# Kernel optimization log

Measured on AMD Instinct MI355X. Metric: run time of the kernel, lower is better.

Reference implementation:

```python
import jax, jax.numpy as jnp
import numpy as np


def setup_inputs() -> dict:
    key = jax.random.key(0)
    k1, k2, k3, k4, k5 = jax.random.split(key, 5)
    B, T, N, F_IN, F_OUT, N_TYPES = 32, 128, 32, 256, 256, 8
    inp = jax.random.normal(k1, (B, T, N, F_IN), dtype=jnp.float32)
    g = jax.random.uniform(k2, (N, N), dtype=jnp.float32)
    node_type_index = jax.random.randint(k3, (N,), 0, N_TYPES, dtype=jnp.int64 if jax.config.read('jax_enable_x64') else jnp.int32)
    weight = jax.random.normal(k4, (N_TYPES, F_OUT, F_IN), dtype=jnp.float32) * (1.0 / np.sqrt(F_IN))
    bias = jax.random.normal(k5, (N_TYPES, F_OUT), dtype=jnp.float32) * 0.01
    return {"input": inp, "g": g, "node_type_index": node_type_index,
            "weight": weight, "bias": bias}


def reference(input, g, node_type_index, weight, bias):
    # Gather per-node weights/biases by node type.
    w = weight[node_type_index]            # [N, out, in]
    b = bias[node_type_index]              # [N, out]
    # Per-node linear: out[..., n, o] = sum_i input[..., n, i] * w[n, o, i]
    out = jnp.einsum('btni,noi->btno', input, w) + b  # [B, T, N, out]
    # Graph aggregation over node dim: g [N, N] @ out [..., N, out]
    out = jnp.einsum('mn,btno->btmo', g, out)
    return out
```

## Files before the change

kernel.cpp:

```cpp
#include <hip/hip_runtime.h>
#include <hip/hip_bf16.h>
#include <stdint.h>

typedef __bf16 bf16x8 __attribute__((ext_vector_type(8)));
typedef __bf16 bf16x4 __attribute__((ext_vector_type(4)));
typedef float f32x4 __attribute__((ext_vector_type(4)));

#define N_NODES 32
#define FDIM 256
#define N_TYPES 8
#define BT_TILE 32
#define TILES 16
#define ROW_B (FDIM * 2)

__device__ __forceinline__ unsigned swz(unsigned byte_off, unsigned row) {
    return byte_off ^ ((row & 7u) << 4);
}
__device__ __forceinline__ void lds_dma16(void* lds, const void* g) {
    __builtin_amdgcn_global_load_lds(
        (const __attribute__((address_space(1))) unsigned int*)g,
        (__attribute__((address_space(3))) unsigned int*)lds, 16, 0, 0);
}

__global__ __launch_bounds__(256) void k0_convert_w(
    const float* __restrict__ w, __bf16* __restrict__ wp)
{
    int idx = blockIdx.x * 256 + threadIdx.x;
    int t = idx >> 16, o = (idx >> 8) & 255, k = idx & 255;
    unsigned L = (unsigned)(o * ROW_B + k * 2) ^ ((o & 7u) << 4);
    wp[(size_t)t * (FDIM * FDIM) + (L >> 1)] = (__bf16)w[idx];
}

__global__ __launch_bounds__(256, 1) void k1_node_gemm(
    const float* __restrict__ input, const __bf16* __restrict__ wp,
    const float* __restrict__ bias, const int* __restrict__ ntype,
    char* __restrict__ outb)
{
    __shared__ __bf16 sW[FDIM * FDIM];
    __shared__ __bf16 sA[2][BT_TILE * FDIM];

    const int tid = threadIdx.x;
    const int n = blockIdx.x >> 3;
    const int base = (blockIdx.x & 7) * (TILES * BT_TILE);
    const int t = ntype[n];

    const int wid = tid >> 6, lane = tid & 63;
    const int lr = lane & 15, lq = lane >> 4;
    const int sr = tid >> 3;
    const int sk = tid & 7;

    char* sWb = (char*)sW;
    char* sA0 = (char*)sA[0];
    char* sA1 = (char*)sA[1];

    const char* wsrc = (const char*)(wp + (size_t)t * (FDIM * FDIM));
#pragma unroll
    for (int j = 0; j < 32; ++j)
        lds_dma16(sWb + j * 4096 + tid * 16, wsrc + j * 4096 + tid * 16);

    float bv[4];
#pragma unroll
    for (int nf = 0; nf < 4; ++nf)
        bv[nf] = bias[t * FDIM + wid * 64 + nf * 16 + lr];

    const char* Abase = (const char*)input
        + ((size_t)(base + sr) * (N_NODES * FDIM) + n * FDIM) * 4 + sk * 16;
    const size_t tile_stride = (size_t)BT_TILE * N_NODES * FDIM * 4;

    float4 av0[8], av1[8];
#pragma unroll
    for (int q = 0; q < 8; ++q)
        av0[q] = *reinterpret_cast<const float4*>(Abase + q * 128);
#pragma unroll
    for (int q = 0; q < 8; ++q)
        av1[q] = *reinterpret_cast<const float4*>(Abase + tile_stride + q * 128);

#pragma unroll
    for (int q = 0; q < 8; ++q) {
        bf16x4 h; h[0]=(__bf16)av0[q].x; h[1]=(__bf16)av0[q].y;
        h[2]=(__bf16)av0[q].z; h[3]=(__bf16)av0[q].w;
        *reinterpret_cast<bf16x4*>(sA0 + swz(sr * ROW_B + q * 64 + sk * 8, sr)) = h;
    }
    __syncthreads();

    f32x4 acc[2][4];

#define COMPUTE_TILE(SBUF, TI)                                                  \
    {                                                                           \
        _Pragma("unroll")                                                       \
        for (int mf = 0; mf < 2; ++mf)                                          \
            _Pragma("unroll")                                                   \
            for (int nf = 0; nf < 4; ++nf)                                      \
                acc[mf][nf] = f32x4{0.f, 0.f, 0.f, 0.f};                        \
        _Pragma("unroll")                                                       \
        for (int ks = 0; ks < 8; ++ks) {                                        \
            const int kb = ks * 64 + lq * 16;                                   \
            bf16x8 af[2], bfv[4];                                               \
            _Pragma("unroll")                                                   \
            for (int mf = 0; mf < 2; ++mf) {                                    \
                int r = mf * 16 + lr;                                           \
                af[mf] = *reinterpret_cast<const bf16x8*>(                      \
                    SBUF + swz(r * ROW_B + kb, r));                             \
            }                                                                   \
            _Pragma("unroll")                                                   \
            for (int nf = 0; nf < 4; ++nf) {                                    \
                int o = wid * 64 + nf * 16 + lr;                                \
                bfv[nf] = *reinterpret_cast<const bf16x8*>(                     \
                    sWb + swz(o * ROW_B + kb, o));                              \
            }                                                                   \
            _Pragma("unroll")                                                   \
            for (int mf = 0; mf < 2; ++mf)                                      \
                _Pragma("unroll")                                               \
                for (int nf = 0; nf < 4; ++nf)                                  \
                    acc[mf][nf] = __builtin_amdgcn_mfma_f32_16x16x32_bf16(      \
                        af[mf], bfv[nf], acc[mf][nf], 0, 0, 0);                 \
        }                                                                       \
                  \
        _Pragma("unroll")                                                       \
        for (int mf = 0; mf < 2; ++mf)                                          \
            _Pragma("unroll")                                                   \
            for (int j = 0; j < 4; ++j) {                                       \
                bf16x4 h;                                                       \
                _Pragma("unroll")                                               \
                for (int nf = 0; nf < 4; ++nf)                                  \
                    h[nf] = (__bf16)(acc[mf][nf][j] + bv[nf]);                  \
                size_t bt = (size_t)(base + (TI) * BT_TILE + mf * 16 + lq * 4 + j); \
                *reinterpret_cast<bf16x4*>(outb + bt * 32768 + n * 512          \
                                           + wid * 128 + lr * 8) = h;           \
            }                                                                   \
    }

#define CVT_TO(AV, SDST)                                                        \
    {                                                                           \
        _Pragma("unroll")                                                       \
        for (int q = 0; q < 8; ++q) {                                           \
            bf16x4 h; h[0]=(__bf16)AV[q].x; h[1]=(__bf16)AV[q].y;               \
            h[2]=(__bf16)AV[q].z; h[3]=(__bf16)AV[q].w;                         \
            *reinterpret_cast<bf16x4*>(SDST + swz(sr * ROW_B + q * 64 + sk * 8, \
                                                  sr)) = h;                     \
        }                                                                       \
    }

#define LOAD_TILE(AV, TI)                                                       \
    {                                                                           \
        const char* rp = Abase + (size_t)(TI) * tile_stride;                    \
        _Pragma("unroll")                                                       \
        for (int q = 0; q < 8; ++q)                                             \
            AV[q] = *reinterpret_cast<const float4*>(rp + q * 128);             \
    }

    for (int tt = 0; tt < 8; ++tt) {
        const int e = 2 * tt;
        if (e + 2 < TILES) LOAD_TILE(av0, e + 2);
        COMPUTE_TILE(sA0, e);
        CVT_TO(av1, sA1);
        __syncthreads();
        const int od = 2 * tt + 1;
        if (od + 2 < TILES) LOAD_TILE(av1, od + 2);
        COMPUTE_TILE(sA1, od);
        if (tt < 7) {
            CVT_TO(av0, sA0);
            __syncthreads();
        }
    }
#undef COMPUTE_TILE
#undef CVT_TO
#undef LOAD_TILE
}

__global__ __launch_bounds__(256) void k2_graph_agg(
    char* __restrict__ outb, const float* __restrict__ g)
{
    const int tid = threadIdx.x;
    const int bt = blockIdx.x;
    const int o = tid;
    const unsigned pb = ((unsigned)(o >> 6) << 7) + ((o & 15u) << 3)
                      + (((o >> 4) & 3u) << 1);

    const char* src = outb + (size_t)bt * 32768 + pb;
    float v[N_NODES];
#pragma unroll
    for (int nn = 0; nn < N_NODES; ++nn) {
        unsigned short hv = *reinterpret_cast<const unsigned short*>(src + nn * 512);
        union { unsigned u; float f; } cv; cv.u = (unsigned)hv << 16;
        v[nn] = cv.f;
    }
    __syncthreads();

    float* dst = (float*)(outb + (size_t)bt * 32768) + o;
#pragma unroll 4
    for (int m = 0; m < N_NODES; ++m) {
        float s = 0.f;
#pragma unroll
        for (int nn = 0; nn < N_NODES; ++nn)
            s = fmaf(g[m * N_NODES + nn], v[nn], s);
        dst[m * FDIM] = s;
    }
}

extern "C" void kernel_launch(void* const* d_in, const int* in_sizes, int n_in,
                              void* d_out, int out_size, void* d_ws, size_t ws_size,
                              hipStream_t stream) {
    const float* input  = (const float*)d_in[0];
    const float* g      = (const float*)d_in[1];
    const int*   ntype  = (const int*)d_in[2];
    const float* weight = (const float*)d_in[3];
    const float* bias   = (const float*)d_in[4];
    char* outb = (char*)d_out;
    __bf16* wp = (__bf16*)d_ws;

    const int BT = in_sizes[0] / (N_NODES * FDIM);

    k0_convert_w<<<N_TYPES * FDIM * FDIM / 256, 256, 0, stream>>>(weight, wp);

    k1_node_gemm<<<N_NODES * 8, 256, 0, stream>>>(input, wp, bias, ntype, outb);

    k2_graph_agg<<<BT, 256, 0, stream>>>(outb, g);
}
```

Measured before the change: 82.92 us.

## Store fp32 node-GEMM intermediate in output and stage g in LDS

The node GEMM now writes its fp32 results straight into the output buffer in natural layout, replacing the packed bf16 intermediate. The graph aggregation kernel reads float2 pairs, handles two BT rows per block, and caches g in shared memory instead of reading it from global memory on every FMA. This doubles the intermediate write and read traffic, since fp32 replaces bf16, but removes the bf16 rounding and gives coalesced vector access. The k1 stores are scalar, strided by 16 floats per lane group, which may coalesce less well than the old bf16x4 stores.

```diff
diff --git a/kernel.cpp b/kernel.cpp
--- a/kernel.cpp
+++ b/kernel.cpp
@@ -34,7 +34,7 @@
 __global__ __launch_bounds__(256, 1) void k1_node_gemm(
     const float* __restrict__ input, const __bf16* __restrict__ wp,
     const float* __restrict__ bias, const int* __restrict__ ntype,
-    char* __restrict__ outb)
+    float* __restrict__ outf)
 {
     __shared__ __bf16 sW[FDIM * FDIM];
     __shared__ __bf16 sA[2][BT_TILE * FDIM];
@@ -115,18 +115,17 @@
                     acc[mf][nf] = __builtin_amdgcn_mfma_f32_16x16x32_bf16(      \
                         af[mf], bfv[nf], acc[mf][nf], 0, 0, 0);                 \
         }                                                                       \
-                  \
+                          \
         _Pragma("unroll")                                                       \
         for (int mf = 0; mf < 2; ++mf)                                          \
             _Pragma("unroll")                                                   \
             for (int j = 0; j < 4; ++j) {                                       \
-                bf16x4 h;                                                       \
+                size_t bt = (size_t)(base + (TI) * BT_TILE + mf * 16 + lq * 4 + j); \
+                float* orow = outf + bt * (N_NODES * FDIM) + n * FDIM           \
+                              + wid * 64 + lr;                                  \
                 _Pragma("unroll")                                               \
                 for (int nf = 0; nf < 4; ++nf)                                  \
-                    h[nf] = (__bf16)(acc[mf][nf][j] + bv[nf]);                  \
-                size_t bt = (size_t)(base + (TI) * BT_TILE + mf * 16 + lq * 4 + j); \
-                *reinterpret_cast<bf16x4*>(outb + bt * 32768 + n * 512          \
-                                           + wid * 128 + lr * 8) = h;           \
+                    orow[nf * 16] = acc[mf][nf][j] + bv[nf];                    \
             }                                                                   \
     }
 
@@ -169,32 +168,32 @@
 }
 
 __global__ __launch_bounds__(256) void k2_graph_agg(
-    char* __restrict__ outb, const float* __restrict__ g)
+    float* __restrict__ out, const float* __restrict__ g)
 {
+    __shared__ float gs[N_NODES * N_NODES];
     const int tid = threadIdx.x;
-    const int bt = blockIdx.x;
-    const int o = tid;
-    const unsigned pb = ((unsigned)(o >> 6) << 7) + ((o & 15u) << 3)
-                      + (((o >> 4) & 3u) << 1);
-
-    const char* src = outb + (size_t)bt * 32768 + pb;
-    float v[N_NODES];
-#pragma unroll
-    for (int nn = 0; nn < N_NODES; ++nn) {
-        unsigned short hv = *reinterpret_cast<const unsigned short*>(src + nn * 512);
-        union { unsigned u; float f; } cv; cv.u = (unsigned)hv << 16;
-        v[nn] = cv.f;
-    }
+    reinterpret_cast<float4*>(gs)[tid] = reinterpret_cast<const float4*>(g)[tid];
+
+    const size_t bt = (size_t)blockIdx.x * 2 + (tid >> 7);
+    const int oc = tid & 127;
+    float2* base = reinterpret_cast<float2*>(out + bt * (N_NODES * FDIM)) + oc;
+
+    float2 v[N_NODES];
+#pragma unroll
+    for (int nn = 0; nn < N_NODES; ++nn)
+        v[nn] = base[nn * (FDIM / 2)];
     __syncthreads();
 
-    float* dst = (float*)(outb + (size_t)bt * 32768) + o;
 #pragma unroll 4
     for (int m = 0; m < N_NODES; ++m) {
-        float s = 0.f;
-#pragma unroll
-        for (int nn = 0; nn < N_NODES; ++nn)
-            s = fmaf(g[m * N_NODES + nn], v[nn], s);
-        dst[m * FDIM] = s;
+        float sx = 0.f, sy = 0.f;
+#pragma unroll
+        for (int nn = 0; nn < N_NODES; ++nn) {
+            float gv = gs[m * N_NODES + nn];
+            sx = fmaf(gv, v[nn].x, sx);
+            sy = fmaf(gv, v[nn].y, sy);
+        }
+        base[m * (FDIM / 2)] = float2{sx, sy};
     }
 }
 
@@ -206,14 +205,14 @@
     const int*   ntype  = (const int*)d_in[2];
     const float* weight = (const float*)d_in[3];
     const float* bias   = (const float*)d_in[4];
-    char* outb = (char*)d_out;
+    float* out = (float*)d_out;
     __bf16* wp = (__bf16*)d_ws;
 
     const int BT = in_sizes[0] / (N_NODES * FDIM);
 
     k0_convert_w<<<N_TYPES * FDIM * FDIM / 256, 256, 0, stream>>>(weight, wp);
 
-    k1_node_gemm<<<N_NODES * 8, 256, 0, stream>>>(input, wp, bias, ntype, outb);
-
-    k2_graph_agg<<<BT, 256, 0, stream>>>(outb, g);
-}
+    k1_node_gemm<<<N_NODES * 8, 256, 0, stream>>>(input, wp, bias, ntype, out);
+
+    k2_graph_agg<<<BT / 2, 256, 0, stream>>>(out, g);
+}
```

New measurement: 105.5 us. 27.3% more time.
